# Optimization experiments

Measured on AMD Instinct MI355X. Metric: run time of the kernel, lower is better.

Reference implementation:

```python
import jax, jax.numpy as jnp
import numpy as np

N = 100000          # nodes
E = 800000          # directed edges (before self-loops)
IN_C = 3
HID = 48            # out_channels per head
HEADS = 4
NUM_LAYERS = 3
NEG_SLOPE = 0.2     # PyG GATv2Conv default negative_slope


def setup_inputs() -> dict:
    key = jax.random.key(0)
    ks = iter(jax.random.split(key, 64))
    inp = {}
    inp["x"] = jax.random.normal(next(ks), (N, IN_C), dtype=jnp.float32)
    inp["edge_index"] = jax.random.randint(next(ks), (2, E), 0, N, dtype=jnp.int32)
    dins = [IN_C] + [HID] * (NUM_LAYERS - 1)
    for l, din in enumerate(dins):
        s = 1.0 / np.sqrt(din)
        inp[f"Wl{l}"] = (jax.random.normal(next(ks), (din, HEADS * HID)) * s).astype(jnp.float32)
        inp[f"bl{l}"] = jnp.zeros((HEADS * HID,), jnp.float32)
        inp[f"Wr{l}"] = (jax.random.normal(next(ks), (din, HEADS * HID)) * s).astype(jnp.float32)
        inp[f"br{l}"] = jnp.zeros((HEADS * HID,), jnp.float32)
        inp[f"att{l}"] = (jax.random.normal(next(ks), (HEADS, HID)) / np.sqrt(HID)).astype(jnp.float32)
        inp[f"b{l}"] = jnp.zeros((HID,), jnp.float32)
    inp["head_w"] = (jax.random.normal(next(ks), (HID, 1)) / np.sqrt(HID)).astype(jnp.float32)
    inp["head_b"] = jnp.full((1,), 0.1, jnp.float32)
    return inp


def _gatv2_layer(x, src, dst, Wl, bl, Wr, br, att, bias):
    # PyG GATv2Conv, concat=False, share_weights=False, eval mode (no dropout).
    # x: [N, din]; src/dst: [E'] with self-loops appended.
    xl = (x @ Wl + bl).reshape(N, HEADS, HID)   # lin_l(x) -> source features
    xr = (x @ Wr + br).reshape(N, HEADS, HID)   # lin_r(x) -> target features
    e = jax.nn.leaky_relu(xl[src] + xr[dst], NEG_SLOPE)      # [E', H, C]
    logits = jnp.einsum('ehc,hc->eh', e, att)                # [E', H]
    # numerically stable per-destination-node softmax over incoming edges
    m = jax.ops.segment_max(logits, dst, num_segments=N)     # [N, H]
    ex = jnp.exp(logits - m[dst])
    denom = jax.ops.segment_sum(ex, dst, num_segments=N)     # [N, H]
    alpha = ex / (denom[dst] + 1e-16)                        # [E', H]
    out = jax.ops.segment_sum(xl[src] * alpha[..., None], dst, num_segments=N)  # [N, H, C]
    return out.mean(axis=1) + bias                           # concat=False -> mean over heads, + bias


def reference(x, edge_index, Wl0, bl0, Wr0, br0, att0, b0,
              Wl1, bl1, Wr1, br1, att1, b1,
              Wl2, bl2, Wr2, br2, att2, b2, head_w, head_b):
    loop = jnp.arange(N, dtype=edge_index.dtype)
    src = jnp.concatenate([edge_index[0], loop])  # add_self_loops=True (PyG default)
    dst = jnp.concatenate([edge_index[1], loop])
    params = [(Wl0, bl0, Wr0, br0, att0, b0),
              (Wl1, bl1, Wr1, br1, att1, b1),
              (Wl2, bl2, Wr2, br2, att2, b2)]
    for p in params:
        x = jax.nn.elu(_gatv2_layer(x, src, dst, *p))  # F.elu; dropout is identity in eval
    out = (x @ head_w + head_b)[:, 0]                  # Linear head, squeeze(-1)
    return jax.nn.softplus(out)                        # output_activation='softplus'
```

## Files before the change

kernel.cpp:

```cpp
#include <hip/hip_runtime.h>
#include <math.h>

#define NN 100000
#define EE 800000
#define NHEADS 4
#define HID 48
#define FDIM (NHEADS * HID)
#define ROWB 384
#define SCAN_CHUNK 2048
#define NBLK ((NN + SCAN_CHUNK - 1) / SCAN_CHUNK)

typedef unsigned int uint;

#if __has_builtin(__builtin_amdgcn_exp2f)
#define EXP2(x) __builtin_amdgcn_exp2f(x)
#else
#define EXP2(x) exp2f(x)
#endif

struct U3 { uint x, y, z; };


__global__ void hist_k(const int* __restrict__ ei, int* __restrict__ cnt) {
    int e = blockIdx.x * blockDim.x + threadIdx.x;
    if (e >= EE) return;
    atomicAdd(&cnt[ei[EE + e]], 1);
}

__global__ void scan1_k(const int* __restrict__ cnt, int* __restrict__ rowptr,
                        int* __restrict__ bsum) {
    __shared__ int lds[256];
    int b = blockIdx.x, t = threadIdx.x;
    int base = b * SCAN_CHUNK + t * 8;
    int v[8], s = 0;
#pragma unroll
    for (int i = 0; i < 8; i++) { v[i] = (base + i < NN) ? cnt[base + i] : 0; s += v[i]; }
    lds[t] = s;
    __syncthreads();
    for (int off = 1; off < 256; off <<= 1) {
        int val = (t >= off) ? lds[t - off] : 0;
        __syncthreads();
        lds[t] += val;
        __syncthreads();
    }
    if (t == 255) bsum[b] = lds[255];
    int run = lds[t] - s;
#pragma unroll
    for (int i = 0; i < 8; i++) {
        if (base + i < NN) rowptr[base + i] = run;
        run += v[i];
    }
}

__global__ void scan2_k(int* __restrict__ bsum) {
    if (threadIdx.x == 0 && blockIdx.x == 0) {
        int acc = 0;
        for (int b = 0; b < NBLK; b++) { int v = bsum[b]; bsum[b] = acc; acc += v; }
    }
}

__global__ void scan3_k(int* __restrict__ rowptr, const int* __restrict__ bsum) {
    int i = blockIdx.x * blockDim.x + threadIdx.x;
    if (i < NN) rowptr[i] += bsum[i / SCAN_CHUNK];
}

__global__ void scatter_k(const int* __restrict__ ei, const int* __restrict__ rowptr,
                          int* __restrict__ fill, int* __restrict__ esrc) {
    int e = blockIdx.x * blockDim.x + threadIdx.x;
    if (e >= EE) return;
    int d = ei[EE + e];
    int pos = rowptr[d] + atomicAdd(&fill[d], 1);
    esrc[pos] = ei[e];
}


__device__ __forceinline__ uint f2bf(float x) {
    uint u = __float_as_uint(x);
    return (u + 0x7FFFu + ((u >> 16) & 1u)) >> 16;
}
__device__ __forceinline__ float bfl(uint u) { return __uint_as_float(u << 16); }
__device__ __forceinline__ float bfh(uint u) { return __uint_as_float(u & 0xFFFF0000u); }

template <int DIN>
__launch_bounds__(192)
__global__ void gemm2_k(const float* __restrict__ x,
                        const float* __restrict__ Wl, const float* __restrict__ bl,
                        const float* __restrict__ Wr, const float* __restrict__ br,
                        uint* __restrict__ xlb, uint* __restrict__ xrb) {
    __shared__ float xs[32][53];
    int t = threadIdx.x;
    int f4 = t % 48, nb = t / 48;
    int node0 = blockIdx.x * 32;

    for (int idx = t; idx < 32 * DIN; idx += 192) {
        int n = idx / DIN, k = idx - n * DIN;
        xs[n][k] = x[(size_t)(node0 + n) * DIN + k];
    }
    __syncthreads();

    float4 accl[8], accr[8];
    {
        float4 bl4 = *(const float4*)(bl + f4 * 4);
        float4 br4 = *(const float4*)(br + f4 * 4);
#pragma unroll
        for (int r = 0; r < 8; r++) { accl[r] = bl4; accr[r] = br4; }
    }

#pragma unroll 4
    for (int k = 0; k < DIN; k++) {
        float4 wl4 = *(const float4*)(Wl + k * FDIM + f4 * 4);
        float4 wr4 = *(const float4*)(Wr + k * FDIM + f4 * 4);
#pragma unroll
        for (int r = 0; r < 8; r++) {
            float xv = xs[nb * 8 + r][k];
            accl[r].x = fmaf(xv, wl4.x, accl[r].x);
            accl[r].y = fmaf(xv, wl4.y, accl[r].y);
            accl[r].z = fmaf(xv, wl4.z, accl[r].z);
            accl[r].w = fmaf(xv, wl4.w, accl[r].w);
            accr[r].x = fmaf(xv, wr4.x, accr[r].x);
            accr[r].y = fmaf(xv, wr4.y, accr[r].y);
            accr[r].z = fmaf(xv, wr4.z, accr[r].z);
            accr[r].w = fmaf(xv, wr4.w, accr[r].w);
        }
    }

#pragma unroll
    for (int r = 0; r < 8; r++) {
        size_t n = (size_t)node0 + nb * 8 + r;
        uint2 pl, pr;
        pl.x = f2bf(accl[r].x) | (f2bf(accl[r].y) << 16);
        pl.y = f2bf(accl[r].z) | (f2bf(accl[r].w) << 16);
        pr.x = f2bf(accr[r].x) | (f2bf(accr[r].y) << 16);
        pr.y = f2bf(accr[r].z) | (f2bf(accr[r].w) << 16);
        *(uint2*)((char*)xlb + n * ROWB + f4 * 8) = pl;
        *(uint2*)((char*)xrb + n * ROWB + f4 * 8) = pr;
    }
}

template <int CTRL>
__device__ __forceinline__ float dpp_add(float x) {
    int v = __builtin_amdgcn_update_dpp(0, __float_as_int(x), CTRL, 0xF, 0xF, true);
    return x + __int_as_float(v);
}
__device__ __forceinline__ float red8(float x) {
    x = dpp_add<0x141>(x);
    x = dpp_add<0x04E>(x);
    x = dpp_add<0x0B1>(x);
    return x;
}

__global__ void gat_node_k(const uint* __restrict__ xlb, const uint* __restrict__ xrb,
                           const int* __restrict__ rowptr, const int* __restrict__ cnt,
                           const int* __restrict__ esrc, const float* __restrict__ att,
                           const float* __restrict__ bias, float* __restrict__ xout) {
    int wid = (blockIdx.x * blockDim.x + threadIdx.x) >> 6;
    int lane = threadIdx.x & 63;
    if (wid >= NN) return;
    int d = wid;
    int half = lane >> 5;
    int hb = lane & 31;
    int h = hb >> 3;
    int j = hb & 7;
    int boff = h * 96 + j * 12;
    int half4 = half << 2;

    const float LOG2E = 1.4426950408889634f;
    const float* ap = att + h * HID + j * 6;
    float w0 = ap[0] * LOG2E, w1 = ap[1] * LOG2E, w2 = ap[2] * LOG2E;
    float w3 = ap[3] * LOG2E, w4 = ap[4] * LOG2E, w5 = ap[5] * LOG2E;

    const char* xlc = (const char*)xlb;
    const char* xrc = (const char*)xrb;

    U3 ur = *(const U3*)(xrc + (size_t)d * ROWB + boff);
    float r0 = bfl(ur.x), r1 = bfh(ur.x), r2 = bfl(ur.y);
    float r3 = bfh(ur.y), r4 = bfl(ur.z), r5 = bfh(ur.z);

    U3 us = *(const U3*)(xlc + (size_t)d * ROWB + boff);
    float a0 = bfl(us.x), a1 = bfh(us.x), a2 = bfl(us.y);
    float a3 = bfh(us.y), a4 = bfl(us.z), a5 = bfh(us.z);
    float v0 = a0 + r0; v0 = fmaxf(v0, 0.2f * v0);
    float v1 = a1 + r1; v1 = fmaxf(v1, 0.2f * v1);
    float v2 = a2 + r2; v2 = fmaxf(v2, 0.2f * v2);
    float v3 = a3 + r3; v3 = fmaxf(v3, 0.2f * v3);
    float v4 = a4 + r4; v4 = fmaxf(v4, 0.2f * v4);
    float v5 = a5 + r5; v5 = fmaxf(v5, 0.2f * v5);
    float lself = red8(fmaf(v0, w0, fmaf(v1, w1, fmaf(v2, w2,
                       fmaf(v3, w3, fmaf(v4, w4, v5 * w5))))));

    float m = half ? -3.0e38f : lself;
    float s = half ? 0.0f : 1.0f;
    float o0 = half ? 0.f : a0, o1 = half ? 0.f : a1, o2 = half ? 0.f : a2;
    float o3 = half ? 0.f : a3, o4 = half ? 0.f : a4, o5 = half ? 0.f : a5;

    int start = rowptr[d], deg = cnt[d];

    for (int cb = 0; cb < deg; cb += 64) {
        int rem = deg - cb; if (rem > 64) rem = 64;
        int my_src = 0;
        if (lane < rem) my_src = esrc[start + cb + lane];
        int npairs = (rem + 1) >> 1;

        int src = __builtin_amdgcn_ds_bpermute(half4, my_src);
        uint off = (uint)src * (uint)ROWB + (uint)boff;
        U3 cur = *(const U3*)(xlc + off);

        for (int i = 0; i + 1 < npairs; i++) {
            int nsrc = __builtin_amdgcn_ds_bpermute(((i + 1) << 3) + half4, my_src);
            uint noff = (uint)nsrc * (uint)ROWB + (uint)boff;
            U3 nxt = *(const U3*)(xlc + noff);

            float ca0 = bfl(cur.x), ca1 = bfh(cur.x), ca2 = bfl(cur.y);
            float ca3 = bfh(cur.y), ca4 = bfl(cur.z), ca5 = bfh(cur.z);
            v0 = ca0 + r0; v0 = fmaxf(v0, 0.2f * v0);
            v1 = ca1 + r1; v1 = fmaxf(v1, 0.2f * v1);
            v2 = ca2 + r2; v2 = fmaxf(v2, 0.2f * v2);
            v3 = ca3 + r3; v3 = fmaxf(v3, 0.2f * v3);
            v4 = ca4 + r4; v4 = fmaxf(v4, 0.2f * v4);
            v5 = ca5 + r5; v5 = fmaxf(v5, 0.2f * v5);
            float l = red8(fmaf(v0, w0, fmaf(v1, w1, fmaf(v2, w2,
                           fmaf(v3, w3, fmaf(v4, w4, v5 * w5))))));
            float mn = fmaxf(m, l);
            float c = EXP2(m - mn);
            float p = EXP2(l - mn);
            s = fmaf(s, c, p);
            o0 = fmaf(o0, c, p * ca0);
            o1 = fmaf(o1, c, p * ca1);
            o2 = fmaf(o2, c, p * ca2);
            o3 = fmaf(o3, c, p * ca3);
            o4 = fmaf(o4, c, p * ca4);
            o5 = fmaf(o5, c, p * ca5);
            m = mn;
            cur = nxt;
        }
        {
            int eid = ((npairs - 1) << 1) + half;
            bool valid = eid < rem;
            float ca0 = bfl(cur.x), ca1 = bfh(cur.x), ca2 = bfl(cur.y);
            float ca3 = bfh(cur.y), ca4 = bfl(cur.z), ca5 = bfh(cur.z);
            v0 = ca0 + r0; v0 = fmaxf(v0, 0.2f * v0);
            v1 = ca1 + r1; v1 = fmaxf(v1, 0.2f * v1);
            v2 = ca2 + r2; v2 = fmaxf(v2, 0.2f * v2);
            v3 = ca3 + r3; v3 = fmaxf(v3, 0.2f * v3);
            v4 = ca4 + r4; v4 = fmaxf(v4, 0.2f * v4);
            v5 = ca5 + r5; v5 = fmaxf(v5, 0.2f * v5);
            float l = red8(fmaf(v0, w0, fmaf(v1, w1, fmaf(v2, w2,
                           fmaf(v3, w3, fmaf(v4, w4, v5 * w5))))));
            float mn = valid ? fmaxf(m, l) : m;
            float p = valid ? EXP2(l - mn) : 0.0f;
            float c = EXP2(m - mn);
            s = fmaf(s, c, p);
            o0 = fmaf(o0, c, p * ca0);
            o1 = fmaf(o1, c, p * ca1);
            o2 = fmaf(o2, c, p * ca2);
            o3 = fmaf(o3, c, p * ca3);
            o4 = fmaf(o4, c, p * ca4);
            o5 = fmaf(o5, c, p * ca5);
            m = mn;
        }
    }

    float m2 = __shfl_xor(m, 32);
    float s2 = __shfl_xor(s, 32);
    float mn = fmaxf(m, m2);
    float c1 = EXP2(m - mn), c2 = EXP2(m2 - mn);
    float sm = fmaf(s, c1, s2 * c2);
    float inv = 1.0f / (sm + 1e-16f);
    float q0 = fmaf(o0, c1, __shfl_xor(o0, 32) * c2) * inv;
    float q1 = fmaf(o1, c1, __shfl_xor(o1, 32) * c2) * inv;
    float q2 = fmaf(o2, c1, __shfl_xor(o2, 32) * c2) * inv;
    float q3 = fmaf(o3, c1, __shfl_xor(o3, 32) * c2) * inv;
    float q4 = fmaf(o4, c1, __shfl_xor(o4, 32) * c2) * inv;
    float q5 = fmaf(o5, c1, __shfl_xor(o5, 32) * c2) * inv;

    q0 += __shfl_xor(q0, 8); q0 += __shfl_xor(q0, 16);
    q1 += __shfl_xor(q1, 8); q1 += __shfl_xor(q1, 16);
    q2 += __shfl_xor(q2, 8); q2 += __shfl_xor(q2, 16);
    q3 += __shfl_xor(q3, 8); q3 += __shfl_xor(q3, 16);
    q4 += __shfl_xor(q4, 8); q4 += __shfl_xor(q4, 16);
    q5 += __shfl_xor(q5, 8); q5 += __shfl_xor(q5, 16);

    if (lane < 8) {
        const float* bp = bias + j * 6;
        float y0 = fmaf(q0, 0.25f, bp[0]);
        float y1 = fmaf(q1, 0.25f, bp[1]);
        float y2 = fmaf(q2, 0.25f, bp[2]);
        float y3 = fmaf(q3, 0.25f, bp[3]);
        float y4 = fmaf(q4, 0.25f, bp[4]);
        float y5 = fmaf(q5, 0.25f, bp[5]);
        y0 = y0 > 0.f ? y0 : (EXP2(y0 * LOG2E) - 1.0f);
        y1 = y1 > 0.f ? y1 : (EXP2(y1 * LOG2E) - 1.0f);
        y2 = y2 > 0.f ? y2 : (EXP2(y2 * LOG2E) - 1.0f);
        y3 = y3 > 0.f ? y3 : (EXP2(y3 * LOG2E) - 1.0f);
        y4 = y4 > 0.f ? y4 : (EXP2(y4 * LOG2E) - 1.0f);
        y5 = y5 > 0.f ? y5 : (EXP2(y5 * LOG2E) - 1.0f);
        float* qo = xout + (size_t)d * HID + j * 6;
        *(float2*)(qo) = make_float2(y0, y1);
        *(float2*)(qo + 2) = make_float2(y2, y3);
        *(float2*)(qo + 4) = make_float2(y4, y5);
    }
}

__global__ void head_k(const float* __restrict__ x, const float* __restrict__ w,
                       const float* __restrict__ hb, float* __restrict__ out) {
    int n = blockIdx.x * blockDim.x + threadIdx.x;
    if (n >= NN) return;
    const float* p = x + (size_t)n * HID;
    float acc = 0.f;
#pragma unroll
    for (int c = 0; c < HID; c++) acc = fmaf(p[c], w[c], acc);
    acc += hb[0];
    out[n] = fmaxf(acc, 0.f) + log1pf(expf(-fabsf(acc)));
}

static inline int cdiv(long a, long b) { return (int)((a + b - 1) / b); }

extern "C" void kernel_launch(void* const* d_in, const int* in_sizes, int n_in,
                              void* d_out, int out_size, void* d_ws, size_t ws_size,
                              hipStream_t stream) {
    const float* x0 = (const float*)d_in[0];
    const int* ei = (const int*)d_in[1];
    const float* Wl[3] = {(const float*)d_in[2], (const float*)d_in[8], (const float*)d_in[14]};
    const float* bl[3] = {(const float*)d_in[3], (const float*)d_in[9], (const float*)d_in[15]};
    const float* Wr[3] = {(const float*)d_in[4], (const float*)d_in[10], (const float*)d_in[16]};
    const float* br[3] = {(const float*)d_in[5], (const float*)d_in[11], (const float*)d_in[17]};
    const float* att[3] = {(const float*)d_in[6], (const float*)d_in[12], (const float*)d_in[18]};
    const float* bb[3] = {(const float*)d_in[7], (const float*)d_in[13], (const float*)d_in[19]};
    const float* hw = (const float*)d_in[20];
    const float* hb = (const float*)d_in[21];

    char* ws = (char*)d_ws;
    uint* xlb = (uint*)ws;      ws += (size_t)NN * ROWB;
    uint* xrb = (uint*)ws;      ws += (size_t)NN * ROWB;
    float* bufA = (float*)ws;   ws += (size_t)NN * HID * 4;
    float* bufB = (float*)ws;   ws += (size_t)NN * HID * 4;
    int* rowptr = (int*)ws;     ws += (size_t)NN * 4;
    int* cnt = (int*)ws;        ws += (size_t)NN * 4;
    int* fill = (int*)ws;       ws += (size_t)NN * 4;
    int* esrc = (int*)ws;       ws += (size_t)EE * 4;
    int* bsum = (int*)ws;       ws += (size_t)NBLK * 4;

    hipMemsetAsync(cnt, 0, (size_t)NN * 4, stream);
    hipMemsetAsync(fill, 0, (size_t)NN * 4, stream);
    hist_k<<<cdiv(EE, 256), 256, 0, stream>>>(ei, cnt);
    scan1_k<<<NBLK, 256, 0, stream>>>(cnt, rowptr, bsum);
    scan2_k<<<1, 64, 0, stream>>>(bsum);
    scan3_k<<<cdiv(NN, 256), 256, 0, stream>>>(rowptr, bsum);
    scatter_k<<<cdiv(EE, 256), 256, 0, stream>>>(ei, rowptr, fill, esrc);

    const float* xin = x0;
    float* bufs[2] = {bufA, bufB};
    for (int l = 0; l < 3; l++) {
        float* xout = bufs[l & 1];
        if (l == 0)
            gemm2_k<3><<<NN / 32, 192, 0, stream>>>(
                xin, Wl[0], bl[0], Wr[0], br[0], xlb, xrb);
        else
            gemm2_k<48><<<NN / 32, 192, 0, stream>>>(
                xin, Wl[l], bl[l], Wr[l], br[l], xlb, xrb);
        gat_node_k<<<cdiv((long)NN * 64, 256), 256, 0, stream>>>(
            xlb, xrb, rowptr, cnt, esrc, att[l], bb[l], xout);
        xin = xout;
    }
    head_k<<<cdiv(NN, 256), 256, 0, stream>>>(xin, hw, hb, (float*)d_out);
}
```

Measured before the change: 460.5 us.

## Use bf16 MFMA GEMM with split-weight precision for hidden layers

Layers 1 and 2 now run their input projections through a matrix-core kernel. The GAT node kernel writes its output as padded bf16 activations, and a prep kernel splits each weight into hi/lo bf16 parts to keep accuracy close to fp32 on the weight side. This replaces the scalar FMA GEMM and halves activation traffic between layers. The cost is an extra memset and the weight-prep kernel, plus bf16 rounding of the activations. The edge loop is also restructured to prefetch the next source index one pair ahead.

Result: slower. 485.9 us (+5.5%).

```diff
diff --git a/kernel.cpp b/kernel.cpp
--- a/kernel.cpp
+++ b/kernel.cpp
@@ -2,15 +2,18 @@
 #include <math.h>
 
 #define NN 100000
+#define NPAD 100032
 #define EE 800000
 #define NHEADS 4
 #define HID 48
 #define FDIM (NHEADS * HID)
 #define ROWB 384
+#define KPAD 64
 #define SCAN_CHUNK 2048
 #define NBLK ((NN + SCAN_CHUNK - 1) / SCAN_CHUNK)
 
 typedef unsigned int uint;
+typedef unsigned short ushort;
 
 #if __has_builtin(__builtin_amdgcn_exp2f)
 #define EXP2(x) __builtin_amdgcn_exp2f(x)
@@ -19,6 +22,9 @@
 #endif
 
 struct U3 { uint x, y, z; };
+
+typedef __attribute__((ext_vector_type(8))) short s16x8;
+typedef __attribute__((ext_vector_type(4))) float f32x4;
 
 
 __global__ void hist_k(const int* __restrict__ ei, int* __restrict__ cnt) {
@@ -81,12 +87,32 @@
 __device__ __forceinline__ float bfl(uint u) { return __uint_as_float(u << 16); }
 __device__ __forceinline__ float bfh(uint u) { return __uint_as_float(u & 0xFFFF0000u); }
 
-template <int DIN>
+__global__ void wprep_k(const float* __restrict__ Wl1, const float* __restrict__ Wr1,
+                        const float* __restrict__ Wl2, const float* __restrict__ Wr2,
+                        ushort* __restrict__ Wt1, ushort* __restrict__ Wt2) {
+    int t = blockIdx.x * blockDim.x + threadIdx.x;
+    if (t >= 2 * KPAD * 384) return;
+    int l = t / (KPAD * 384);
+    int rem = t - l * (KPAD * 384);
+    int k = rem / 384;
+    int c = rem - k * 384;
+    int cc = (c >= 192) ? c - 192 : c;
+    const float* W = (l == 0) ? (c < 192 ? Wl1 : Wr1) : (c < 192 ? Wl2 : Wr2);
+    float v = (k < 48) ? W[k * FDIM + cc] : 0.0f;
+    uint hi = f2bf(v);
+    float lo = v - bfl(hi);
+    uint lob = f2bf(lo);
+    ushort* Wt = (l == 0) ? Wt1 : Wt2;
+    Wt[c * KPAD + k] = (ushort)hi;
+    Wt[384 * KPAD + c * KPAD + k] = (ushort)lob;
+}
+
 __launch_bounds__(192)
 __global__ void gemm2_k(const float* __restrict__ x,
                         const float* __restrict__ Wl, const float* __restrict__ bl,
                         const float* __restrict__ Wr, const float* __restrict__ br,
                         uint* __restrict__ xlb, uint* __restrict__ xrb) {
+    const int DIN = 3;
     __shared__ float xs[32][53];
     int t = threadIdx.x;
     int f4 = t % 48, nb = t / 48;
@@ -106,7 +132,7 @@
         for (int r = 0; r < 8; r++) { accl[r] = bl4; accr[r] = br4; }
     }
 
-#pragma unroll 4
+#pragma unroll
     for (int k = 0; k < DIN; k++) {
         float4 wl4 = *(const float4*)(Wl + k * FDIM + f4 * 4);
         float4 wr4 = *(const float4*)(Wr + k * FDIM + f4 * 4);
@@ -137,6 +163,65 @@
     }
 }
 
+__launch_bounds__(256)
+__global__ void gemm_mfma_k(const ushort* __restrict__ xbf,
+                            const ushort* __restrict__ Wt,
+                            const float* __restrict__ bl, const float* __restrict__ br,
+                            ushort* __restrict__ xlb, ushort* __restrict__ xrb) {
+    __shared__ ushort cs[64 * 96];
+    int cg = blockIdx.x & 3;
+    int n0 = (blockIdx.x >> 2) * 64;
+    int wave = threadIdx.x >> 6, lane = threadIdx.x & 63;
+    int l15 = lane & 15, l16 = lane >> 4;
+    int arow = n0 + wave * 16 + l15;
+    int k8 = l16 * 8;
+
+    const ushort* ap = xbf + (size_t)arow * KPAD + k8;
+    s16x8 a0 = *(const s16x8*)(ap);
+    s16x8 a1 = *(const s16x8*)(ap + 32);
+
+    f32x4 acc[6];
+#pragma unroll
+    for (int ct = 0; ct < 6; ct++) {
+        int cglob = cg * 96 + ct * 16 + l15;
+        float bv = (cglob < 192) ? bl[cglob] : br[cglob - 192];
+        acc[ct] = (f32x4){bv, bv, bv, bv};
+        const ushort* bp = Wt + (size_t)cglob * KPAD + k8;
+        s16x8 bh0 = *(const s16x8*)(bp);
+        s16x8 bh1 = *(const s16x8*)(bp + 32);
+        s16x8 bl0 = *(const s16x8*)(bp + 384 * KPAD);
+        s16x8 bl1 = *(const s16x8*)(bp + 384 * KPAD + 32);
+        acc[ct] = __builtin_amdgcn_mfma_f32_16x16x32_bf16(a0, bh0, acc[ct], 0, 0, 0);
+        acc[ct] = __builtin_amdgcn_mfma_f32_16x16x32_bf16(a1, bh1, acc[ct], 0, 0, 0);
+        acc[ct] = __builtin_amdgcn_mfma_f32_16x16x32_bf16(a0, bl0, acc[ct], 0, 0, 0);
+        acc[ct] = __builtin_amdgcn_mfma_f32_16x16x32_bf16(a1, bl1, acc[ct], 0, 0, 0);
+    }
+
+#pragma unroll
+    for (int ct = 0; ct < 6; ct++) {
+#pragma unroll
+        for (int r = 0; r < 4; r++) {
+            int row = wave * 16 + l16 * 4 + r;
+            cs[row * 96 + ct * 16 + l15] = (ushort)f2bf(acc[ct][r]);
+        }
+    }
+    __syncthreads();
+
+    int colbase = cg * 96;
+    ushort* outm = (colbase < 192) ? xlb : xrb;
+    int cb = (colbase >= 192) ? colbase - 192 : colbase;
+#pragma unroll
+    for (int i = 0; i < 3; i++) {
+        int idx = threadIdx.x + i * 256;
+        int row = idx / 12, q = idx - row * 12;
+        int node = n0 + row;
+        if (node < NN) {
+            uint4 v = *(const uint4*)(&cs[row * 96 + q * 8]);
+            *(uint4*)(outm + (size_t)node * FDIM + cb + q * 8) = v;
+        }
+    }
+}
+
 template <int CTRL>
 __device__ __forceinline__ float dpp_add(float x) {
     int v = __builtin_amdgcn_update_dpp(0, __float_as_int(x), CTRL, 0xF, 0xF, true);
@@ -149,10 +234,36 @@
     return x;
 }
 
+#define GAT_PAIR(CU, VALID)                                                      \
+    {                                                                            \
+        float ca0 = bfl(CU.x), ca1 = bfh(CU.x), ca2 = bfl(CU.y);                 \
+        float ca3 = bfh(CU.y), ca4 = bfl(CU.z), ca5 = bfh(CU.z);                 \
+        float t0 = ca0 + r0; t0 = fmaxf(t0, 0.2f * t0);                          \
+        float t1 = ca1 + r1; t1 = fmaxf(t1, 0.2f * t1);                          \
+        float t2 = ca2 + r2; t2 = fmaxf(t2, 0.2f * t2);                          \
+        float t3 = ca3 + r3; t3 = fmaxf(t3, 0.2f * t3);                          \
+        float t4 = ca4 + r4; t4 = fmaxf(t4, 0.2f * t4);                          \
+        float t5 = ca5 + r5; t5 = fmaxf(t5, 0.2f * t5);                          \
+        float l = red8(fmaf(t0, w0, fmaf(t1, w1, fmaf(t2, w2,                    \
+                       fmaf(t3, w3, fmaf(t4, w4, t5 * w5))))));                  \
+        float mn = (VALID) ? fmaxf(m, l) : m;                                    \
+        float p = (VALID) ? EXP2(l - mn) : 0.0f;                                 \
+        float c = EXP2(m - mn);                                                  \
+        s = fmaf(s, c, p);                                                       \
+        o0 = fmaf(o0, c, p * ca0);                                               \
+        o1 = fmaf(o1, c, p * ca1);                                               \
+        o2 = fmaf(o2, c, p * ca2);                                               \
+        o3 = fmaf(o3, c, p * ca3);                                               \
+        o4 = fmaf(o4, c, p * ca4);                                               \
+        o5 = fmaf(o5, c, p * ca5);                                               \
+        m = mn;                                                                  \
+    }
+
 __global__ void gat_node_k(const uint* __restrict__ xlb, const uint* __restrict__ xrb,
                            const int* __restrict__ rowptr, const int* __restrict__ cnt,
                            const int* __restrict__ esrc, const float* __restrict__ att,
-                           const float* __restrict__ bias, float* __restrict__ xout) {
+                           const float* __restrict__ bias,
+                           ushort* __restrict__ xbf_out, float* __restrict__ xf_out) {
     int wid = (blockIdx.x * blockDim.x + threadIdx.x) >> 6;
     int lane = threadIdx.x & 63;
     if (wid >= NN) return;
@@ -201,62 +312,19 @@
         if (lane < rem) my_src = esrc[start + cb + lane];
         int npairs = (rem + 1) >> 1;
 
-        int src = __builtin_amdgcn_ds_bpermute(half4, my_src);
-        uint off = (uint)src * (uint)ROWB + (uint)boff;
-        U3 cur = *(const U3*)(xlc + off);
-
-        for (int i = 0; i + 1 < npairs; i++) {
-            int nsrc = __builtin_amdgcn_ds_bpermute(((i + 1) << 3) + half4, my_src);
-            uint noff = (uint)nsrc * (uint)ROWB + (uint)boff;
-            U3 nxt = *(const U3*)(xlc + noff);
-
-            float ca0 = bfl(cur.x), ca1 = bfh(cur.x), ca2 = bfl(cur.y);
-            float ca3 = bfh(cur.y), ca4 = bfl(cur.z), ca5 = bfh(cur.z);
-            v0 = ca0 + r0; v0 = fmaxf(v0, 0.2f * v0);
-            v1 = ca1 + r1; v1 = fmaxf(v1, 0.2f * v1);
-            v2 = ca2 + r2; v2 = fmaxf(v2, 0.2f * v2);
-            v3 = ca3 + r3; v3 = fmaxf(v3, 0.2f * v3);
-            v4 = ca4 + r4; v4 = fmaxf(v4, 0.2f * v4);
-            v5 = ca5 + r5; v5 = fmaxf(v5, 0.2f * v5);
-            float l = red8(fmaf(v0, w0, fmaf(v1, w1, fmaf(v2, w2,
-                           fmaf(v3, w3, fmaf(v4, w4, v5 * w5))))));
-            float mn = fmaxf(m, l);
-            float c = EXP2(m - mn);
-            float p = EXP2(l - mn);
-            s = fmaf(s, c, p);
-            o0 = fmaf(o0, c, p * ca0);
-            o1 = fmaf(o1, c, p * ca1);
-            o2 = fmaf(o2, c, p * ca2);
-            o3 = fmaf(o3, c, p * ca3);
-            o4 = fmaf(o4, c, p * ca4);
-            o5 = fmaf(o5, c, p * ca5);
-            m = mn;
+        int sA = __builtin_amdgcn_ds_bpermute(half4, my_src);
+        int sB = __builtin_amdgcn_ds_bpermute(8 + half4, my_src);
+        U3 cur = *(const U3*)(xlc + (uint)sA * (uint)ROWB + (uint)boff);
+
+        for (int i = 0; i < npairs - 1; i++) {
+            U3 nxt = *(const U3*)(xlc + (uint)sB * (uint)ROWB + (uint)boff);
+            sB = __builtin_amdgcn_ds_bpermute(((i + 2) << 3) + half4, my_src);
+            GAT_PAIR(cur, true);
             cur = nxt;
         }
         {
-            int eid = ((npairs - 1) << 1) + half;
-            bool valid = eid < rem;
-            float ca0 = bfl(cur.x), ca1 = bfh(cur.x), ca2 = bfl(cur.y);
-            float ca3 = bfh(cur.y), ca4 = bfl(cur.z), ca5 = bfh(cur.z);
-            v0 = ca0 + r0; v0 = fmaxf(v0, 0.2f * v0);
-            v1 = ca1 + r1; v1 = fmaxf(v1, 0.2f * v1);
-            v2 = ca2 + r2; v2 = fmaxf(v2, 0.2f * v2);
-            v3 = ca3 + r3; v3 = fmaxf(v3, 0.2f * v3);
-            v4 = ca4 + r4; v4 = fmaxf(v4, 0.2f * v4);
-            v5 = ca5 + r5; v5 = fmaxf(v5, 0.2f * v5);
-            float l = red8(fmaf(v0, w0, fmaf(v1, w1, fmaf(v2, w2,
-                           fmaf(v3, w3, fmaf(v4, w4, v5 * w5))))));
-            float mn = valid ? fmaxf(m, l) : m;
-            float p = valid ? EXP2(l - mn) : 0.0f;
-            float c = EXP2(m - mn);
-            s = fmaf(s, c, p);
-            o0 = fmaf(o0, c, p * ca0);
-            o1 = fmaf(o1, c, p * ca1);
-            o2 = fmaf(o2, c, p * ca2);
-            o3 = fmaf(o3, c, p * ca3);
-            o4 = fmaf(o4, c, p * ca4);
-            o5 = fmaf(o5, c, p * ca5);
-            m = mn;
+            bool valid = (((npairs - 1) << 1) + half) < rem;
+            GAT_PAIR(cur, valid);
         }
     }
 
@@ -294,10 +362,19 @@
         y3 = y3 > 0.f ? y3 : (EXP2(y3 * LOG2E) - 1.0f);
         y4 = y4 > 0.f ? y4 : (EXP2(y4 * LOG2E) - 1.0f);
         y5 = y5 > 0.f ? y5 : (EXP2(y5 * LOG2E) - 1.0f);
-        float* qo = xout + (size_t)d * HID + j * 6;
-        *(float2*)(qo) = make_float2(y0, y1);
-        *(float2*)(qo + 2) = make_float2(y2, y3);
-        *(float2*)(qo + 4) = make_float2(y4, y5);
+        if (xbf_out) {
+            U3 pk;
+            pk.x = f2bf(y0) | (f2bf(y1) << 16);
+            pk.y = f2bf(y2) | (f2bf(y3) << 16);
+            pk.z = f2bf(y4) | (f2bf(y5) << 16);
+            *(U3*)(xbf_out + (size_t)d * KPAD + j * 6) = pk;
+        }
+        if (xf_out) {
+            float* qo = xf_out + (size_t)d * HID + j * 6;
+            *(float2*)(qo) = make_float2(y0, y1);
+            *(float2*)(qo + 2) = make_float2(y2, y3);
+            *(float2*)(qo + 4) = make_float2(y4, y5);
+        }
     }
 }
 
@@ -333,7 +410,9 @@
     uint* xlb = (uint*)ws;      ws += (size_t)NN * ROWB;
     uint* xrb = (uint*)ws;      ws += (size_t)NN * ROWB;
     float* bufA = (float*)ws;   ws += (size_t)NN * HID * 4;
-    float* bufB = (float*)ws;   ws += (size_t)NN * HID * 4;
+    ushort* xbf = (ushort*)ws;  ws += (size_t)NPAD * KPAD * 2;
+    ushort* Wt1 = (ushort*)ws;  ws += (size_t)2 * 384 * KPAD * 2;
+    ushort* Wt2 = (ushort*)ws;  ws += (size_t)2 * 384 * KPAD * 2;
     int* rowptr = (int*)ws;     ws += (size_t)NN * 4;
     int* cnt = (int*)ws;        ws += (size_t)NN * 4;
     int* fill = (int*)ws;       ws += (size_t)NN * 4;
@@ -342,25 +421,28 @@
 
     hipMemsetAsync(cnt, 0, (size_t)NN * 4, stream);
     hipMemsetAsync(fill, 0, (size_t)NN * 4, stream);
+    hipMemsetAsync(xbf, 0, (size_t)NPAD * KPAD * 2, stream);
+    wprep_k<<<cdiv(2 * KPAD * 384, 256), 256, 0, stream>>>(Wl[1], Wr[1], Wl[2], Wr[2], Wt1, Wt2);
     hist_k<<<cdiv(EE, 256), 256, 0, stream>>>(ei, cnt);
     scan1_k<<<NBLK, 256, 0, stream>>>(cnt, rowptr, bsum);
     scan2_k<<<1, 64, 0, stream>>>(bsum);
     scan3_k<<<cdiv(NN, 256), 256, 0, stream>>>(rowptr, bsum);
     scatter_k<<<cdiv(EE, 256), 256, 0, stream>>>(ei, rowptr, fill, esrc);
 
-    const float* xin = x0;
-    float* bufs[2] = {bufA, bufB};
-    for (int l = 0; l < 3; l++) {
-        float* xout = bufs[l & 1];
-        if (l == 0)
-            gemm2_k<3><<<NN / 32, 192, 0, stream>>>(
-                xin, Wl[0], bl[0], Wr[0], br[0], xlb, xrb);
-        else
-            gemm2_k<48><<<NN / 32, 192, 0, stream>>>(
-                xin, Wl[l], bl[l], Wr[l], br[l], xlb, xrb);
-        gat_node_k<<<cdiv((long)NN * 64, 256), 256, 0, stream>>>(
-            xlb, xrb, rowptr, cnt, esrc, att[l], bb[l], xout);
-        xin = xout;
-    }
-    head_k<<<cdiv(NN, 256), 256, 0, stream>>>(xin, hw, hb, (float*)d_out);
-}
+    const int GAT_GRID = cdiv((long)NN * 64, 256);
+    const int MFMA_GRID = cdiv(NN, 64) * 4;
+
+    gemm2_k<<<NN / 32, 192, 0, stream>>>(x0, Wl[0], bl[0], Wr[0], br[0], xlb, xrb);
+    gat_node_k<<<GAT_GRID, 256, 0, stream>>>(xlb, xrb, rowptr, cnt, esrc, att[0], bb[0],
+                                             xbf, (float*)nullptr);
+    gemm_mfma_k<<<MFMA_GRID, 256, 0, stream>>>(xbf, Wt1, bl[1], br[1],
+                                               (ushort*)xlb, (ushort*)xrb);
+    gat_node_k<<<GAT_GRID, 256, 0, stream>>>(xlb, xrb, rowptr, cnt, esrc, att[1], bb[1],
+                                             xbf, (float*)nullptr);
+    gemm_mfma_k<<<MFMA_GRID, 256, 0, stream>>>(xbf, Wt2, bl[2], br[2],
+                                               (ushort*)xlb, (ushort*)xrb);
+    gat_node_k<<<GAT_GRID, 256, 0, stream>>>(xlb, xrb, rowptr, cnt, esrc, att[2], bb[2],
+                                             (ushort*)nullptr, bufA);
+
+    head_k<<<cdiv(NN, 256), 256, 0, stream>>>(bufA, hw, hb, (float*)d_out);
+}
```
